# Performance work log

Measured on AMD Instinct MI355X. Metric: run time of the kernel, lower is better.

## Reference

```python
import jax, jax.numpy as jnp
import numpy as np

N_NODES = 100000


def gcn_layer(x, W, b, src, dst, norm, n):
    # x: [N, Fin] -> linear transform then normalized scatter-add aggregation
    h = x @ W                                   # [N, Fout]
    msgs = h[src] * norm[:, None]               # [E+N, Fout] edge messages
    out = jax.ops.segment_sum(msgs, dst, num_segments=n)
    return out + b


def _build_graph(edge_index, n):
    # add self loops (PyG GCNConv default)
    loops = jnp.arange(n, dtype=edge_index.dtype)
    src = jnp.concatenate([edge_index[0], loops])
    dst = jnp.concatenate([edge_index[1], loops])
    deg = jax.ops.segment_sum(jnp.ones_like(dst, dtype=jnp.float32), dst, num_segments=n)
    dis = jnp.where(deg > 0, jax.lax.rsqrt(deg), 0.0)  # deg^{-1/2}
    norm = dis[src] * dis[dst]                  # symmetric normalization per edge
    return src, dst, norm


def setup_inputs() -> dict:
    key = jax.random.key(0)
    ks = jax.random.split(key, 8)
    x = jax.random.normal(ks[0], (N_NODES, 3), dtype=jnp.float32)
    edge_index = jax.random.randint(ks[1], (2, 6400000), 0, N_NODES, dtype=jnp.int32)
    def glorot(k, fin, fout):
        s = jnp.sqrt(6.0 / (fin + fout))
        return jax.random.uniform(k, (fin, fout), jnp.float32, -s, s)
    return {
        "x": x,
        "edge_index": edge_index,
        "W1": glorot(ks[2], 3, 32), "b1": jnp.zeros((32,), jnp.float32),
        "W2": glorot(ks[3], 32, 32), "b2": jnp.zeros((32,), jnp.float32),
        "W3": glorot(ks[4], 32, 1), "b3": jnp.zeros((1,), jnp.float32),
    }


def reference(x, edge_index, W1, b1, W2, b2, W3, b3):
    n = x.shape[0]
    src, dst, norm = _build_graph(edge_index, n)
    h = jax.nn.relu(gcn_layer(x, W1, b1, src, dst, norm, n))
    h = jax.nn.relu(gcn_layer(h, W2, b2, src, dst, norm, n))
    return gcn_layer(h, W3, b3, src, dst, norm, n)
```

## Files before the change

### kernel.cpp

```cpp
#include <hip/hip_runtime.h>
#include <hip/hip_fp16.h>


#define BLK 256
#define BLK2 512
#define SB 1600
#define CHUNK 4000
#define BKT 128
#define NBKT 782
#define MAXNB 1024
#define BUFSZ 9950

__global__ void k_hist(const int* __restrict__ dst, int* __restrict__ hist, int E) {
    __shared__ int lh[NBKT];
    for (int b = threadIdx.x; b < NBKT; b += blockDim.x) lh[b] = 0;
    __syncthreads();
    int beg = blockIdx.x * CHUNK;
    int end = min(E, beg + CHUNK);
    int nq = (end - beg) >> 2;
    const int4* d4 = (const int4*)(dst + beg);
    for (int i = threadIdx.x; i < nq; i += blockDim.x) {
        int4 d = d4[i];
        atomicAdd(&lh[d.x >> 7], 1);
        atomicAdd(&lh[d.y >> 7], 1);
        atomicAdd(&lh[d.z >> 7], 1);
        atomicAdd(&lh[d.w >> 7], 1);
    }
    for (int e = beg + (nq << 2) + threadIdx.x; e < end; e += blockDim.x)
        atomicAdd(&lh[dst[e] >> 7], 1);
    __syncthreads();
    for (int b = threadIdx.x; b < NBKT; b += blockDim.x)
        hist[(size_t)blockIdx.x * NBKT + b] = lh[b];
}

__global__ void k_scanA(int* __restrict__ hist, int* __restrict__ btot, int NB) {
    int b = blockIdx.x, t = threadIdx.x;
    int base = t * 4;
    int v0 = (base + 0 < SB) ? hist[(size_t)(base + 0) * NB + b] : 0;
    int v1 = (base + 1 < SB) ? hist[(size_t)(base + 1) * NB + b] : 0;
    int v2 = (base + 2 < SB) ? hist[(size_t)(base + 2) * NB + b] : 0;
    int v3 = (base + 3 < SB) ? hist[(size_t)(base + 3) * NB + b] : 0;
    int s = v0 + v1 + v2 + v3;
    int lane = t & 63, w = t >> 6;
    int x = s;
#pragma unroll
    for (int off = 1; off < 64; off <<= 1) {
        int u = __shfl_up(x, off, 64);
        if (lane >= off) x += u;
    }
    __shared__ int wsum[8];
    if (lane == 63) wsum[w] = x;
    __syncthreads();
    int woff = 0;
    for (int k = 0; k < 8; k++) woff += (k < w) ? wsum[k] : 0;
    int run = woff + x - s;
    if (base + 0 < SB) hist[(size_t)(base + 0) * NB + b] = run;  run += v0;
    if (base + 1 < SB) hist[(size_t)(base + 1) * NB + b] = run;  run += v1;
    if (base + 2 < SB) hist[(size_t)(base + 2) * NB + b] = run;  run += v2;
    if (base + 3 < SB) hist[(size_t)(base + 3) * NB + b] = run;  run += v3;
    if (t == 511) btot[b] = run;
}

__global__ void k_scanB(const int* __restrict__ btot, int* __restrict__ bbase,
                        int NB, int E) {
    __shared__ int sh[MAXNB];
    int t = threadIdx.x;
    int v = (t < NB) ? btot[t] : 0;
    sh[t] = v;
    __syncthreads();
    for (int off = 1; off < MAXNB; off <<= 1) {
        int u = (t >= off) ? sh[t - off] : 0;
        __syncthreads();
        sh[t] += u;
        __syncthreads();
    }
    if (t < NB) bbase[t] = sh[t] - v;
    if (t == 0) bbase[NB] = E;
}

__global__ void k_bsort(const int* __restrict__ src, const int* __restrict__ dst,
                        const int* __restrict__ hist, const int* __restrict__ btot,
                        const int* __restrict__ bbase,
                        unsigned int* __restrict__ packed, int E) {
    __shared__ unsigned int bufB[CHUNK];
    __shared__ unsigned short binarr2[CHUNK];
    __shared__ int cnt[NBKT];
    __shared__ int off[NBKT];
    __shared__ int cur[NBKT];
    __shared__ int gbase[NBKT];
    __shared__ int wsum[8];
    int t = threadIdx.x;
    int beg = blockIdx.x * CHUNK;
    int end = min(E, beg + CHUNK);
    int len = end - beg;
    int last = (blockIdx.x + 1 == gridDim.x);
    for (int b = t; b < NBKT; b += blockDim.x) {
        int my = hist[(size_t)blockIdx.x * NBKT + b];
        int nx = last ? btot[b] : hist[(size_t)(blockIdx.x + 1) * NBKT + b];
        cnt[b] = nx - my;
        gbase[b] = bbase[b] + my;
    }
    __syncthreads();
    {
        int base = t * 2;
        int v0 = (base + 0 < NBKT) ? cnt[base + 0] : 0;
        int v1 = (base + 1 < NBKT) ? cnt[base + 1] : 0;
        int s = v0 + v1;
        int lane = t & 63, w = t >> 6;
        int x = s;
#pragma unroll
        for (int o = 1; o < 64; o <<= 1) {
            int u = __shfl_up(x, o, 64);
            if (lane >= o) x += u;
        }
        if (lane == 63) wsum[w] = x;
        __syncthreads();
        int woff = 0;
        for (int k = 0; k < 8; k++) woff += (k < w) ? wsum[k] : 0;
        int run = woff + x - s;
        if (base + 0 < NBKT) { off[base + 0] = run; cur[base + 0] = run; } run += v0;
        if (base + 1 < NBKT) { off[base + 1] = run; cur[base + 1] = run; } run += v1;
    }
    __syncthreads();
    for (int i = t; i < len; i += blockDim.x) {
        int d = dst[beg + i];
        int s = src[beg + i];
        int b = d >> 7;
        int pos = atomicAdd(&cur[b], 1);
        bufB[pos] = (unsigned)s | ((unsigned)(d & 127) << 17);
        binarr2[pos] = (unsigned short)b;
    }
    __syncthreads();
    for (int i = t; i < len; i += blockDim.x) {
        int b = binarr2[i];
        packed[gbase[b] + i - off[b]] = bufB[i];
    }
}

__global__ void k_sort(unsigned int* __restrict__ packed, const int* __restrict__ bbase,
                       const float* __restrict__ x, float* __restrict__ dis,
                       float4* __restrict__ y4, int* __restrict__ rowptr, int N, int E) {
    __shared__ unsigned int buf[BUFSZ];
    __shared__ int cnt[BKT];
    __shared__ int cur[BKT];
    __shared__ int wsum[2];
    int b = blockIdx.x, t = threadIdx.x;
    int beg = bbase[b], end = bbase[b + 1];
    int len = end - beg;
    if (t < BKT) cnt[t] = 0;
    __syncthreads();
    for (int i = t; i < len; i += blockDim.x) {
        unsigned v = packed[beg + i];
        buf[i] = v;
        atomicAdd(&cnt[v >> 17], 1);
    }
    __syncthreads();
    int v0 = 0, xs = 0;
    if (t < BKT) {
        v0 = cnt[t];
        xs = v0;
#pragma unroll
        for (int o = 1; o < 64; o <<= 1) {
            int u = __shfl_up(xs, o, 64);
            if ((t & 63) >= o) xs += u;
        }
        if ((t & 63) == 63) wsum[t >> 6] = xs;
    }
    __syncthreads();
    if (t < BKT) {
        int woff = (t >= 64) ? wsum[0] : 0;
        int excl = woff + xs - v0;
        cur[t] = excl;
        int gi = b * BKT + t;
        if (gi < N) {
            rowptr[gi] = beg + excl;
            float di = rsqrtf((float)v0 + 1.0f);
            dis[gi] = di;
            float4 y;
            y.x = di * x[3 * gi + 0];
            y.y = di * x[3 * gi + 1];
            y.z = di * x[3 * gi + 2];
            y.w = 0.0f;
            y4[gi] = y;
        }
    }
    __syncthreads();
    for (int i = t; i < len; i += blockDim.x) {
        unsigned vv = buf[i];
        int pos = atomicAdd(&cur[vv >> 17], 1);
        packed[beg + pos] = vv & 0x1FFFF;
    }
    if (b == 0 && t == 0) rowptr[N] = E;
}

__global__ void k_l1(const unsigned int* __restrict__ csr, const int* __restrict__ rowptr,
                     const float4* __restrict__ y4, const float* __restrict__ dis,
                     const float* __restrict__ W1, const float* __restrict__ b1,
                     __half* __restrict__ g, int N) {
    int t = blockIdx.x * blockDim.x + threadIdx.x;
    int i = t >> 5, j = t & 31;
    if (i >= N) return;
    int beg = rowptr[i], end = rowptr[i + 1];
    float ax = 0.f, ay = 0.f, az = 0.f;
    for (int e = beg + j; e < end; e += 32) {
        float4 yv = y4[csr[e]];
        ax += yv.x; ay += yv.y; az += yv.z;
    }
#pragma unroll
    for (int m = 16; m >= 1; m >>= 1) {
        ax += __shfl_xor(ax, m, 32);
        ay += __shfl_xor(ay, m, 32);
        az += __shfl_xor(az, m, 32);
    }
    float di = dis[i];
    float4 ys = y4[i];
    float a0 = di * (ax + ys.x);
    float a1 = di * (ay + ys.y);
    float a2 = di * (az + ys.z);
    float h = b1[j] + a0 * W1[j] + a1 * W1[32 + j] + a2 * W1[64 + j];
    g[(size_t)i * 32 + j] = __float2half(di * fmaxf(h, 0.f));
}

__device__ __forceinline__ void acc4(float& c0, float& c1, float& c2, float& c3,
                                     uint2 r) {
    __half2 a = *(const __half2*)&r.x;
    __half2 b = *(const __half2*)&r.y;
    float2 fa = __half22float2(a);
    float2 fb = __half22float2(b);
    c0 += fa.x; c1 += fa.y; c2 += fb.x; c3 += fb.y;
}

__global__ void k_l2(const unsigned int* __restrict__ csr, const int* __restrict__ rowptr,
                     const __half* __restrict__ g, const float* __restrict__ dis,
                     const float* __restrict__ W2, const float* __restrict__ b2,
                     const float* __restrict__ W3, float* __restrict__ q, int N) {
    __shared__ float sW2[1024];
    __shared__ float sb2[32];
    __shared__ float sW3[32];
    int tid = threadIdx.x;
    ((float4*)sW2)[tid] = ((const float4*)W2)[tid];
    if (tid < 32) { sb2[tid] = b2[tid]; sW3[tid] = W3[tid]; }
    __syncthreads();
    int t = blockIdx.x * blockDim.x + tid;
    int i = t >> 3, j = t & 7;
    if (i >= N) return;
    int beg = rowptr[i], end = rowptr[i + 1];
    const uint2* g2 = (const uint2*)g;
    float pa0 = 0.f, pa1 = 0.f, pa2 = 0.f, pa3 = 0.f;
    float pb0 = 0.f, pb1 = 0.f, pb2 = 0.f, pb3 = 0.f;
    float pc0 = 0.f, pc1 = 0.f, pc2 = 0.f, pc3 = 0.f;
    float pd0 = 0.f, pd1 = 0.f, pd2 = 0.f, pd3 = 0.f;
    int e = beg;
    for (; e < end && (e & 3); e++) {
        int s = (int)csr[e];
        uint2 r = g2[s * 8 + j];
        acc4(pa0, pa1, pa2, pa3, r);
    }
    for (; e + 8 <= end; e += 8) {
        int4 ca = *(const int4*)(csr + e);
        int4 cb = *(const int4*)(csr + e + 4);
        uint2 r0 = g2[ca.x * 8 + j];
        uint2 r1 = g2[ca.y * 8 + j];
        uint2 r2 = g2[ca.z * 8 + j];
        uint2 r3 = g2[ca.w * 8 + j];
        uint2 r4 = g2[cb.x * 8 + j];
        uint2 r5 = g2[cb.y * 8 + j];
        uint2 r6 = g2[cb.z * 8 + j];
        uint2 r7 = g2[cb.w * 8 + j];
        acc4(pa0, pa1, pa2, pa3, r0);
        acc4(pb0, pb1, pb2, pb3, r1);
        acc4(pc0, pc1, pc2, pc3, r2);
        acc4(pd0, pd1, pd2, pd3, r3);
        acc4(pa0, pa1, pa2, pa3, r4);
        acc4(pb0, pb1, pb2, pb3, r5);
        acc4(pc0, pc1, pc2, pc3, r6);
        acc4(pd0, pd1, pd2, pd3, r7);
    }
    for (; e < end; e++) {
        int s = (int)csr[e];
        uint2 r = g2[s * 8 + j];
        acc4(pa0, pa1, pa2, pa3, r);
    }
    float c0 = (pa0 + pb0) + (pc0 + pd0);
    float c1 = (pa1 + pb1) + (pc1 + pd1);
    float c2 = (pa2 + pb2) + (pc2 + pd2);
    float c3 = (pa3 + pb3) + (pc3 + pd3);
    float di = dis[i];
    uint2 rs = g2[i * 8 + j];
    float2 sa = __half22float2(*(const __half2*)&rs.x);
    float2 sb = __half22float2(*(const __half2*)&rs.y);
    float a0 = di * (c0 + sa.x);
    float a1 = di * (c1 + sa.y);
    float a2 = di * (c2 + sb.x);
    float a3 = di * (c3 + sb.y);
    int m = 4 * j;
    float4 bo = *(const float4*)&sb2[m];
    float o0 = bo.x, o1 = bo.y, o2 = bo.z, o3 = bo.w;
#pragma unroll
    for (int kl = 0; kl < 8; kl++) {
        float x0 = __shfl(a0, kl, 8);
        float x1 = __shfl(a1, kl, 8);
        float x2 = __shfl(a2, kl, 8);
        float x3 = __shfl(a3, kl, 8);
        float4 w0 = *(const float4*)&sW2[(4 * kl + 0) * 32 + m];
        float4 w1 = *(const float4*)&sW2[(4 * kl + 1) * 32 + m];
        float4 w2 = *(const float4*)&sW2[(4 * kl + 2) * 32 + m];
        float4 w3 = *(const float4*)&sW2[(4 * kl + 3) * 32 + m];
        o0 = fmaf(x0, w0.x, fmaf(x1, w1.x, fmaf(x2, w2.x, fmaf(x3, w3.x, o0))));
        o1 = fmaf(x0, w0.y, fmaf(x1, w1.y, fmaf(x2, w2.y, fmaf(x3, w3.y, o1))));
        o2 = fmaf(x0, w0.z, fmaf(x1, w1.z, fmaf(x2, w2.z, fmaf(x3, w3.z, o2))));
        o3 = fmaf(x0, w0.w, fmaf(x1, w1.w, fmaf(x2, w2.w, fmaf(x3, w3.w, o3))));
    }
    float4 wv = *(const float4*)&sW3[m];
    float cc = fmaxf(o0, 0.f) * wv.x + fmaxf(o1, 0.f) * wv.y
             + fmaxf(o2, 0.f) * wv.z + fmaxf(o3, 0.f) * wv.w;
    cc += __shfl_xor(cc, 1, 8);
    cc += __shfl_xor(cc, 2, 8);
    cc += __shfl_xor(cc, 4, 8);
    if (j == 0) q[i] = di * cc;
}

__global__ void k_l3(const unsigned int* __restrict__ csr, const int* __restrict__ rowptr,
                     const float* __restrict__ q, const float* __restrict__ dis,
                     const float* __restrict__ b3, float* __restrict__ out, int N) {
    int t = blockIdx.x * blockDim.x + threadIdx.x;
    int i = t >> 5, j = t & 31;
    if (i >= N) return;
    int beg = rowptr[i], end = rowptr[i + 1];
    float acc = 0.f;
    for (int e = beg + j; e < end; e += 32)
        acc += q[csr[e]];
#pragma unroll
    for (int m = 16; m >= 1; m >>= 1)
        acc += __shfl_xor(acc, m, 32);
    if (j == 0) out[i] = dis[i] * (acc + q[i]) + b3[0];
}

extern "C" void kernel_launch(void* const* d_in, const int* in_sizes, int n_in,
                              void* d_out, int out_size, void* d_ws, size_t ws_size,
                              hipStream_t stream) {
    const float* x  = (const float*)d_in[0];
    const int*   ei = (const int*)d_in[1];
    const float* W1 = (const float*)d_in[2];
    const float* b1 = (const float*)d_in[3];
    const float* W2 = (const float*)d_in[4];
    const float* b2 = (const float*)d_in[5];
    const float* W3 = (const float*)d_in[6];
    const float* b3 = (const float*)d_in[7];
    float* out = (float*)d_out;

    int N = in_sizes[0] / 3;
    int E = in_sizes[1] / 2;
    const int* src = ei;
    const int* dst = ei + E;

    char* w = (char*)d_ws;
#define CARVE(nbytes) w; w += (((size_t)(nbytes) + 255) & ~(size_t)255)
    int*   hist   = (int*)  CARVE((size_t)SB * NBKT * 4);
    int*   btot   = (int*)  CARVE((size_t)MAXNB * 4);
    int*   bbase  = (int*)  CARVE((size_t)(MAXNB + 1) * 4);
    int*   rowptr = (int*)  CARVE((size_t)(N + 1) * 4);
    float* dis    = (float*)CARVE((size_t)N * 4);
    float* y4     = (float*)CARVE((size_t)N * 16);
    __half* g     = (__half*)CARVE((size_t)N * 32 * 2);
    float* q      = (float*)CARVE((size_t)N * 4);
    unsigned int* packed = (unsigned int*)CARVE((size_t)E * 4);
#undef CARVE

    k_hist <<<SB, BLK, 0, stream>>>(dst, hist, E);
    k_scanA<<<NBKT, BLK2, 0, stream>>>(hist, btot, NBKT);
    k_scanB<<<1, MAXNB, 0, stream>>>(btot, bbase, NBKT, E);
    k_bsort<<<SB, BLK2, 0, stream>>>(src, dst, hist, btot, bbase, packed, E);
    k_sort <<<NBKT, BLK2, 0, stream>>>(packed, bbase, x, dis, (float4*)y4, rowptr, N, E);

    long long tn = (long long)N * 32;
    unsigned gn = (unsigned)((tn + BLK - 1) / BLK);
    long long tn8 = (long long)N * 8;
    unsigned gn8 = (unsigned)((tn8 + BLK - 1) / BLK);
    k_l1<<<gn,  BLK, 0, stream>>>(packed, rowptr, (const float4*)y4, dis, W1, b1, g, N);
    k_l2<<<gn8, BLK, 0, stream>>>(packed, rowptr, g, dis, W2, b2, W3, q, N);
    k_l3<<<gn,  BLK, 0, stream>>>(packed, rowptr, q, dis, b3, out, N);
}
```

Measured before the change: 326.7 us.

## Quantize layer-1 features to per-node uint8 and input features to fp16

Layer-1 output features move from fp16 to uint8, using a per-node max scale computed with a warp reduction, so each 32-wide row takes 32 bytes. The scaled input features move from float4 to packed half4. Both changes cut gather traffic in the edge loops of k_l1 and k_l2. In exchange each gathered row needs an extra scale load and integer-to-float unpacking, and 8-bit quantization adds error that may exceed the accuracy tolerance.

```diff
diff --git a/kernel.cpp b/kernel.cpp
--- a/kernel.cpp
+++ b/kernel.cpp
@@ -139,7 +139,7 @@
 
 __global__ void k_sort(unsigned int* __restrict__ packed, const int* __restrict__ bbase,
                        const float* __restrict__ x, float* __restrict__ dis,
-                       float4* __restrict__ y4, int* __restrict__ rowptr, int N, int E) {
+                       uint2* __restrict__ y8, int* __restrict__ rowptr, int N, int E) {
     __shared__ unsigned int buf[BUFSZ];
     __shared__ int cnt[BKT];
     __shared__ int cur[BKT];
@@ -176,12 +176,11 @@
             rowptr[gi] = beg + excl;
             float di = rsqrtf((float)v0 + 1.0f);
             dis[gi] = di;
-            float4 y;
-            y.x = di * x[3 * gi + 0];
-            y.y = di * x[3 * gi + 1];
-            y.z = di * x[3 * gi + 2];
-            y.w = 0.0f;
-            y4[gi] = y;
+            uint2 yv;
+            *(__half2*)&yv.x = __floats2half2_rn(di * x[3 * gi + 0],
+                                                 di * x[3 * gi + 1]);
+            *(__half2*)&yv.y = __floats2half2_rn(di * x[3 * gi + 2], 0.f);
+            y8[gi] = yv;
         }
     }
     __syncthreads();
@@ -194,17 +193,19 @@
 }
 
 __global__ void k_l1(const unsigned int* __restrict__ csr, const int* __restrict__ rowptr,
-                     const float4* __restrict__ y4, const float* __restrict__ dis,
+                     const uint2* __restrict__ y8, const float* __restrict__ dis,
                      const float* __restrict__ W1, const float* __restrict__ b1,
-                     __half* __restrict__ g, int N) {
+                     unsigned char* __restrict__ gi8, float* __restrict__ gs, int N) {
     int t = blockIdx.x * blockDim.x + threadIdx.x;
     int i = t >> 5, j = t & 31;
     if (i >= N) return;
     int beg = rowptr[i], end = rowptr[i + 1];
     float ax = 0.f, ay = 0.f, az = 0.f;
     for (int e = beg + j; e < end; e += 32) {
-        float4 yv = y4[csr[e]];
-        ax += yv.x; ay += yv.y; az += yv.z;
+        uint2 v = y8[csr[e]];
+        float2 fa = __half22float2(*(const __half2*)&v.x);
+        float2 fb = __half22float2(*(const __half2*)&v.y);
+        ax += fa.x; ay += fa.y; az += fb.x;
     }
 #pragma unroll
     for (int m = 16; m >= 1; m >>= 1) {
@@ -213,25 +214,34 @@
         az += __shfl_xor(az, m, 32);
     }
     float di = dis[i];
-    float4 ys = y4[i];
-    float a0 = di * (ax + ys.x);
-    float a1 = di * (ay + ys.y);
-    float a2 = di * (az + ys.z);
+    uint2 vs = y8[i];
+    float2 sa = __half22float2(*(const __half2*)&vs.x);
+    float2 sb = __half22float2(*(const __half2*)&vs.y);
+    float a0 = di * (ax + sa.x);
+    float a1 = di * (ay + sa.y);
+    float a2 = di * (az + sb.x);
     float h = b1[j] + a0 * W1[j] + a1 * W1[32 + j] + a2 * W1[64 + j];
-    g[(size_t)i * 32 + j] = __float2half(di * fmaxf(h, 0.f));
-}
-
-__device__ __forceinline__ void acc4(float& c0, float& c1, float& c2, float& c3,
-                                     uint2 r) {
-    __half2 a = *(const __half2*)&r.x;
-    __half2 b = *(const __half2*)&r.y;
-    float2 fa = __half22float2(a);
-    float2 fb = __half22float2(b);
-    c0 += fa.x; c1 += fa.y; c2 += fb.x; c3 += fb.y;
+    float val = di * fmaxf(h, 0.f);
+    float mv = val;
+#pragma unroll
+    for (int m = 16; m >= 1; m >>= 1)
+        mv = fmaxf(mv, __shfl_xor(mv, m, 32));
+    float inv = (mv > 0.f) ? 255.0f / mv : 0.f;
+    gi8[(size_t)i * 32 + j] = (unsigned char)__float2uint_rn(val * inv);
+    if (j == 0) gs[i] = mv * (1.0f / 255.0f);
+}
+
+__device__ __forceinline__ void accq(float& c0, float& c1, float& c2, float& c3,
+                                     unsigned r, float sc) {
+    c0 = fmaf(sc, (float)(r & 0xffu), c0);
+    c1 = fmaf(sc, (float)((r >> 8) & 0xffu), c1);
+    c2 = fmaf(sc, (float)((r >> 16) & 0xffu), c2);
+    c3 = fmaf(sc, (float)(r >> 24), c3);
 }
 
 __global__ void k_l2(const unsigned int* __restrict__ csr, const int* __restrict__ rowptr,
-                     const __half* __restrict__ g, const float* __restrict__ dis,
+                     const unsigned int* __restrict__ gi4, const float* __restrict__ gs,
+                     const float* __restrict__ dis,
                      const float* __restrict__ W2, const float* __restrict__ b2,
                      const float* __restrict__ W3, float* __restrict__ q, int N) {
     __shared__ float sW2[1024];
@@ -245,7 +255,6 @@
     int i = t >> 3, j = t & 7;
     if (i >= N) return;
     int beg = rowptr[i], end = rowptr[i + 1];
-    const uint2* g2 = (const uint2*)g;
     float pa0 = 0.f, pa1 = 0.f, pa2 = 0.f, pa3 = 0.f;
     float pb0 = 0.f, pb1 = 0.f, pb2 = 0.f, pb3 = 0.f;
     float pc0 = 0.f, pc1 = 0.f, pc2 = 0.f, pc3 = 0.f;
@@ -253,46 +262,43 @@
     int e = beg;
     for (; e < end && (e & 3); e++) {
         int s = (int)csr[e];
-        uint2 r = g2[s * 8 + j];
-        acc4(pa0, pa1, pa2, pa3, r);
+        accq(pa0, pa1, pa2, pa3, gi4[s * 8 + j], gs[s]);
     }
     for (; e + 8 <= end; e += 8) {
         int4 ca = *(const int4*)(csr + e);
         int4 cb = *(const int4*)(csr + e + 4);
-        uint2 r0 = g2[ca.x * 8 + j];
-        uint2 r1 = g2[ca.y * 8 + j];
-        uint2 r2 = g2[ca.z * 8 + j];
-        uint2 r3 = g2[ca.w * 8 + j];
-        uint2 r4 = g2[cb.x * 8 + j];
-        uint2 r5 = g2[cb.y * 8 + j];
-        uint2 r6 = g2[cb.z * 8 + j];
-        uint2 r7 = g2[cb.w * 8 + j];
-        acc4(pa0, pa1, pa2, pa3, r0);
-        acc4(pb0, pb1, pb2, pb3, r1);
-        acc4(pc0, pc1, pc2, pc3, r2);
-        acc4(pd0, pd1, pd2, pd3, r3);
-        acc4(pa0, pa1, pa2, pa3, r4);
-        acc4(pb0, pb1, pb2, pb3, r5);
-        acc4(pc0, pc1, pc2, pc3, r6);
-        acc4(pd0, pd1, pd2, pd3, r7);
+        unsigned r0 = gi4[ca.x * 8 + j]; float s0 = gs[ca.x];
+        unsigned r1 = gi4[ca.y * 8 + j]; float s1 = gs[ca.y];
+        unsigned r2 = gi4[ca.z * 8 + j]; float s2 = gs[ca.z];
+        unsigned r3 = gi4[ca.w * 8 + j]; float s3 = gs[ca.w];
+        unsigned r4 = gi4[cb.x * 8 + j]; float s4 = gs[cb.x];
+        unsigned r5 = gi4[cb.y * 8 + j]; float s5 = gs[cb.y];
+        unsigned r6 = gi4[cb.z * 8 + j]; float s6 = gs[cb.z];
+        unsigned r7 = gi4[cb.w * 8 + j]; float s7 = gs[cb.w];
+        accq(pa0, pa1, pa2, pa3, r0, s0);
+        accq(pb0, pb1, pb2, pb3, r1, s1);
+        accq(pc0, pc1, pc2, pc3, r2, s2);
+        accq(pd0, pd1, pd2, pd3, r3, s3);
+        accq(pa0, pa1, pa2, pa3, r4, s4);
+        accq(pb0, pb1, pb2, pb3, r5, s5);
+        accq(pc0, pc1, pc2, pc3, r6, s6);
+        accq(pd0, pd1, pd2, pd3, r7, s7);
     }
     for (; e < end; e++) {
         int s = (int)csr[e];
-        uint2 r = g2[s * 8 + j];
-        acc4(pa0, pa1, pa2, pa3, r);
+        accq(pa0, pa1, pa2, pa3, gi4[s * 8 + j], gs[s]);
     }
     float c0 = (pa0 + pb0) + (pc0 + pd0);
     float c1 = (pa1 + pb1) + (pc1 + pd1);
     float c2 = (pa2 + pb2) + (pc2 + pd2);
     float c3 = (pa3 + pb3) + (pc3 + pd3);
     float di = dis[i];
-    uint2 rs = g2[i * 8 + j];
-    float2 sa = __half22float2(*(const __half2*)&rs.x);
-    float2 sb = __half22float2(*(const __half2*)&rs.y);
-    float a0 = di * (c0 + sa.x);
-    float a1 = di * (c1 + sa.y);
-    float a2 = di * (c2 + sb.x);
-    float a3 = di * (c3 + sb.y);
+    unsigned rs = gi4[i * 8 + j];
+    float ssc = gs[i];
+    float a0 = di * (c0 + ssc * (float)(rs & 0xffu));
+    float a1 = di * (c1 + ssc * (float)((rs >> 8) & 0xffu));
+    float a2 = di * (c2 + ssc * (float)((rs >> 16) & 0xffu));
+    float a3 = di * (c3 + ssc * (float)(rs >> 24));
     int m = 4 * j;
     float4 bo = *(const float4*)&sb2[m];
     float o0 = bo.x, o1 = bo.y, o2 = bo.z, o3 = bo.w;
@@ -361,8 +367,9 @@
     int*   bbase  = (int*)  CARVE((size_t)(MAXNB + 1) * 4);
     int*   rowptr = (int*)  CARVE((size_t)(N + 1) * 4);
     float* dis    = (float*)CARVE((size_t)N * 4);
-    float* y4     = (float*)CARVE((size_t)N * 16);
-    __half* g     = (__half*)CARVE((size_t)N * 32 * 2);
+    uint2* y8     = (uint2*)CARVE((size_t)N * 8);
+    unsigned char* gi8 = (unsigned char*)CARVE((size_t)N * 32);
+    float* gs     = (float*)CARVE((size_t)N * 4);
     float* q      = (float*)CARVE((size_t)N * 4);
     unsigned int* packed = (unsigned int*)CARVE((size_t)E * 4);
 #undef CARVE
@@ -371,13 +378,14 @@
     k_scanA<<<NBKT, BLK2, 0, stream>>>(hist, btot, NBKT);
     k_scanB<<<1, MAXNB, 0, stream>>>(btot, bbase, NBKT, E);
     k_bsort<<<SB, BLK2, 0, stream>>>(src, dst, hist, btot, bbase, packed, E);
-    k_sort <<<NBKT, BLK2, 0, stream>>>(packed, bbase, x, dis, (float4*)y4, rowptr, N, E);
+    k_sort <<<NBKT, BLK2, 0, stream>>>(packed, bbase, x, dis, y8, rowptr, N, E);
 
     long long tn = (long long)N * 32;
     unsigned gn = (unsigned)((tn + BLK - 1) / BLK);
     long long tn8 = (long long)N * 8;
     unsigned gn8 = (unsigned)((tn8 + BLK - 1) / BLK);
-    k_l1<<<gn,  BLK, 0, stream>>>(packed, rowptr, (const float4*)y4, dis, W1, b1, g, N);
-    k_l2<<<gn8, BLK, 0, stream>>>(packed, rowptr, g, dis, W2, b2, W3, q, N);
+    k_l1<<<gn,  BLK, 0, stream>>>(packed, rowptr, y8, dis, W1, b1, gi8, gs, N);
+    k_l2<<<gn8, BLK, 0, stream>>>(packed, rowptr, (const unsigned int*)gi8, gs,
+                                  dis, W2, b2, W3, q, N);
     k_l3<<<gn,  BLK, 0, stream>>>(packed, rowptr, q, dis, b3, out, N);
 }
```

Result: no change. 330.6 us (+1.2%).
